# Optimization experiments

Measured on AMD Instinct MI355X. Metric: run time of the kernel, lower is better.

## Reference

```python
import jax, jax.numpy as jnp
import numpy as np

D_MODEL = 1024
NUM_HEADS = 16
HEAD_DIM = D_MODEL // NUM_HEADS
THETA = 10000.0
MAX_SEQ_LEN = 2048
BATCH = 4
SEQ = 2048


def _rope_tables():
    # theta_vec = 1 / theta**(arange(0, d_k, 2)/d_k), pos outer product
    inv_freq = 1.0 / (THETA ** (jnp.arange(0, HEAD_DIM, 2, dtype=jnp.float32) / HEAD_DIM))
    pos = jnp.arange(MAX_SEQ_LEN, dtype=jnp.float32)
    freqs = jnp.outer(pos, inv_freq)  # [max_seq, head_dim//2]
    return jnp.cos(freqs), jnp.sin(freqs)


def apply_rope(x, cos, sin):
    # x: [..., S, d]; cos/sin: [S, d//2]; interleaved pairwise rotation
    x1 = x[..., 0::2]
    x2 = x[..., 1::2]
    o1 = x1 * cos - x2 * sin
    o2 = x2 * cos + x1 * sin
    return jnp.stack([o1, o2], axis=-1).reshape(x.shape)


def setup_inputs() -> dict:
    key = jax.random.key(0)
    kx, kq, kk, kv, ko = jax.random.split(key, 5)
    std = (1.0 / D_MODEL) ** 0.5
    x = jax.random.normal(kx, (BATCH, SEQ, D_MODEL), dtype=jnp.float32)
    w_q = jax.random.normal(kq, (D_MODEL, D_MODEL), dtype=jnp.float32) * std
    w_k = jax.random.normal(kk, (D_MODEL, D_MODEL), dtype=jnp.float32) * std
    w_v = jax.random.normal(kv, (D_MODEL, D_MODEL), dtype=jnp.float32) * std
    w_o = jax.random.normal(ko, (D_MODEL, D_MODEL), dtype=jnp.float32) * std
    cos, sin = _rope_tables()
    return {"x": x, "w_q": w_q, "w_k": w_k, "w_v": w_v, "w_o": w_o,
            "cos": cos, "sin": sin}


def reference(x, w_q, w_k, w_v, w_o, cos, sin):
    b, s, d = x.shape
    h, dk = NUM_HEADS, HEAD_DIM

    def proj(w):
        # einsum '... s d, hd d -> ... s hd' == x @ w.T, then split heads
        y = jnp.einsum('bsd,ed->bse', x, w)
        return y.reshape(b, s, h, dk).transpose(0, 2, 1, 3)  # [b,h,s,dk]

    q = apply_rope(proj(w_q), cos[:s], sin[:s])
    k = apply_rope(proj(w_k), cos[:s], sin[:s])
    v = proj(w_v)

    scores = jnp.einsum('bhnd,bhmd->bhnm', q, k) / (dk ** 0.5)
    causal = jnp.tril(jnp.ones((s, s), dtype=bool))
    scores = jnp.where(causal, scores, -jnp.inf)
    attn = jax.nn.softmax(scores, axis=-1)
    out = jnp.einsum('bhnm,bhmd->bhnd', attn, v)  # [b,h,s,dk]
    out = out.transpose(0, 2, 1, 3).reshape(b, s, d)
    # einsum '... s hd, d hd -> ... s d' == out @ w_o.T
    return jnp.einsum('bse,de->bsd', out, w_o)
```

## Files before the change

### kernel.cpp

```cpp
#include <hip/hip_runtime.h>
#include <hip/hip_bf16.h>


typedef __bf16 bf16;
typedef __bf16 bf16x8 __attribute__((ext_vector_type(8)));
typedef __bf16 bf16x4 __attribute__((ext_vector_type(4)));
typedef float f32x4 __attribute__((ext_vector_type(4)));

#define LOG2E 1.4426950408889634f
#define QSCALE (0.125f * LOG2E * 8388608.0f)
#define SEXP_SEED ((126.94269504f - 16.0f * LOG2E) * 8388608.0f)

__device__ __forceinline__ void async16(const void* g, void* l) {
  __builtin_amdgcn_global_load_lds(
      (const __attribute__((address_space(1))) void*)g,
      (__attribute__((address_space(3))) void*)l, 16, 0, 0);
}

#define MFMA16(a, b, c) __builtin_amdgcn_mfma_f32_16x16x32_bf16(a, b, c, 0, 0, 0)

__global__ void cast_all_kernel(const float* __restrict__ x,
                                const float* __restrict__ wq,
                                const float* __restrict__ wk,
                                const float* __restrict__ wv,
                                const float* __restrict__ wo,
                                const float* __restrict__ cosT,
                                const float* __restrict__ sinT,
                                bf16* __restrict__ xb, bf16* __restrict__ wb,
                                float2* __restrict__ csT) {
  int i = blockIdx.x * blockDim.x + threadIdx.x;
  if (i >= 3145728) {
    int j = i - 3145728;
    float2 cs;
    cs.x = cosT[j];
    cs.y = sinT[j];
    csT[j] = cs;
    return;
  }
  const float* src;
  bf16* dst;
  long o;
  if (i < 2097152) {
    src = x; dst = xb; o = i;
  } else {
    long j = i - 2097152;
    int w = (int)(j >> 18);
    o = j & 262143;
    src = (w == 0) ? wq : (w == 1) ? wk : (w == 2) ? wv : wo;
    dst = wb + (long)w * 1048576;
  }
  float4 v = reinterpret_cast<const float4*>(src)[o];
  bf16x4 out;
  out.x = (bf16)v.x; out.y = (bf16)v.y; out.z = (bf16)v.z; out.w = (bf16)v.w;
  *reinterpret_cast<bf16x4*>(dst + o * 4) = out;
}

template <int EPI, int TM, int TN>
__device__ __forceinline__ void gemm_dev(const bf16* __restrict__ A,
                                         const bf16* __restrict__ B,
                                         void* __restrict__ C, int N, int K,
                                         int bm, int bn, bf16* As, bf16* Bs,
                                         const float2* __restrict__ csT) {
  constexpr int WM = TM / 64;
  constexpr int WN = 4 / WM;
  constexpr int CW = TN / WN;
  constexpr int NT = CW / 16;
  constexpr int ROUNDS = (TM + TN) / 64;
  const int tid = threadIdx.x;
  const int wid = tid >> 6, lane = tid & 63;
  const int quad = lane >> 4, l15 = lane & 15;
  const int waveM = wid / WN, waveN = wid % WN;

  f32x4 acc[4][NT] = {};
  const bf16* Ag = A + (long)bm * TM * K;
  const bf16* Bg = B + (long)bn * TN * K;

  auto stage = [&](int buf, int k0) {
#pragma unroll
    for (int ri = 0; ri < ROUNDS; ++ri) {
      int c = ri * 256 + tid;
      int g = ri * 256 + (wid << 6);
      bool isA = g < TM * 4;
      int cl = isA ? c : c - TM * 4;
      int r = cl >> 2;
      int col = ((cl & 3) ^ ((r >> 1) & 3)) << 3;
      const bf16* src = (isA ? Ag : Bg) + (long)r * K + k0 + col;
      char* dst = isA ? ((char*)As + (long)buf * (TM * 64) + (long)g * 16)
                      : ((char*)Bs + (long)buf * (TN * 64) +
                         (long)(g - TM * 4) * 16);
      async16(src, dst);
    }
  };

  stage(0, 0);
  __syncthreads();
  int cur = 0;
  for (int k0 = 0; k0 < K; k0 += 32) {
    const bool more = (k0 + 32) < K;
    if (more) stage(cur ^ 1, k0 + 32);
    const bf16* Asb = As + cur * (TM * 32);
    const bf16* Bsb = Bs + cur * (TN * 32);
    bf16x8 af[4], bfr[NT];
#pragma unroll
    for (int t = 0; t < 4; ++t) {
      int rowA = waveM * 64 + t * 16 + l15;
      af[t] =
          *(const bf16x8*)(Asb + rowA * 32 + ((quad ^ ((rowA >> 1) & 3)) << 3));
    }
#pragma unroll
    for (int t = 0; t < NT; ++t) {
      int rowB = waveN * CW + t * 16 + l15;
      bfr[t] =
          *(const bf16x8*)(Bsb + rowB * 32 + ((quad ^ ((rowB >> 1) & 3)) << 3));
    }
#pragma unroll
    for (int mt = 0; mt < 4; ++mt)
#pragma unroll
      for (int nt = 0; nt < NT; ++nt)
        acc[mt][nt] = MFMA16(af[mt], bfr[nt], acc[mt][nt]);
    if (more) {
      __syncthreads();
      cur ^= 1;
    }
  }

  const float qsc = (EPI == 0 && bn < 8) ? QSCALE : 1.0f;
#pragma unroll
  for (int mt = 0; mt < 4; ++mt)
#pragma unroll
    for (int nt = 0; nt < NT; ++nt)
#pragma unroll
      for (int r = 0; r < 4; ++r) {
        int row = bm * TM + waveM * 64 + mt * 16 + quad * 4 + r;
        int col = bn * TN + waveN * CW + nt * 16 + l15;
        float v = acc[mt][nt][r];
        if (EPI == 0) {
          float pr = __shfl_xor(v, 1);
          int d = col & 63;
          float2 cs = csT[(row & 2047) * 32 + (d >> 1)];
          float o =
              (col & 1) ? (v * cs.x + pr * cs.y) : (v * cs.x - pr * cs.y);
          o *= qsc;
          long off = (long)(col >> 10) * 8388608 +
                     (long)(((row >> 11) << 4) + ((col >> 6) & 15)) * 131072 +
                     (long)(row & 2047) * 64 + d;
          ((bf16*)C)[off] = (bf16)o;
        } else if (EPI == 1) {
          long off = (long)(col >> 11) * 2097152 + (long)row * 2048 +
                     (col & 2047);
          ((bf16*)C)[off] = (bf16)v;
        } else {
          ((float*)C)[(long)row * N + col] = v;
        }
      }
}

__global__ __launch_bounds__(256) void gemm_qkv(const bf16* __restrict__ xb,
                                                const bf16* __restrict__ wqk,
                                                const bf16* __restrict__ wv,
                                                bf16* __restrict__ QK,
                                                bf16* __restrict__ VT,
                                                const float2* __restrict__ csT) {
  __shared__ __align__(16) bf16 As[2 * 128 * 32];
  __shared__ __align__(16) bf16 Bs[2 * 128 * 32];
  int p = blockIdx.x;
  if (p >= 1024) {
    int pv = p - 1024;
    int lv = (pv & 7) * 128 + (pv >> 3);
    gemm_dev<1, 64, 128>(wv, xb, VT, 8192, 1024, lv & 15, lv >> 4, As, Bs,
                         nullptr);
  } else {
    int l = (p & 7) * 128 + (p >> 3);
    gemm_dev<0, 128, 128>(xb, wqk, QK, 2048, 1024, l >> 4, l & 15, As, Bs,
                          csT);
  }
}

__global__ __launch_bounds__(256) void gemm_out(const bf16* __restrict__ A,
                                                const bf16* __restrict__ B,
                                                float* __restrict__ C) {
  __shared__ __align__(16) bf16 As[2 * 128 * 32];
  __shared__ __align__(16) bf16 Bs[2 * 64 * 32];
  gemm_dev<2, 128, 64>(A, B, C, 1024, 1024, blockIdx.y, blockIdx.x, As, Bs,
                       nullptr);
}

__device__ __forceinline__ void attn_step(const bf16* Ks, const bf16* Vs,
                                          bf16* Pw, const bf16x8* qf,
                                          const bf16x8 ones, f32x4* accO,
                                          f32x4& accL, int quad, int l15,
                                          int qloc, bool diag) {
  const int sw = l15 & 7;
  const f32x4 seedv = {SEXP_SEED, SEXP_SEED, SEXP_SEED, SEXP_SEED};
  f32x4 sacc[4] = {seedv, seedv, seedv, seedv};
#pragma unroll
  for (int mt = 0; mt < 4; ++mt)
#pragma unroll
    for (int kk = 0; kk < 2; ++kk) {
      bf16x8 kf = *(const bf16x8*)(Ks + (mt * 16 + l15) * 64 +
                                   ((((kk << 2) + quad) ^ sw) << 3));
      sacc[mt] = MFMA16(kf, qf[kk], sacc[mt]);
    }
  if (diag) {
#pragma unroll
    for (int mt = 0; mt < 4; ++mt)
#pragma unroll
      for (int r = 0; r < 4; ++r)
        if ((mt * 16 + quad * 4 + r) > qloc) sacc[mt][r] = 0.0f;
  }
#pragma unroll
  for (int mt = 0; mt < 4; ++mt) {
    int i0 = (int)sacc[mt][0], i1 = (int)sacc[mt][1];
    int i2 = (int)sacc[mt][2], i3 = (int)sacc[mt][3];
    uint2 pk;
    pk.x = __builtin_amdgcn_perm((unsigned)i1, (unsigned)i0, 0x07060302u);
    pk.y = __builtin_amdgcn_perm((unsigned)i3, (unsigned)i2, 0x07060302u);
    *(uint2*)(Pw + l15 * 88 + mt * 16 + quad * 4) = pk;
  }
  asm volatile("s_waitcnt lgkmcnt(0)" ::: "memory");
  bf16x8 pfr[2];
#pragma unroll
  for (int kk = 0; kk < 2; ++kk)
    pfr[kk] = *(const bf16x8*)(Pw + l15 * 88 + kk * 32 + quad * 8);
#pragma unroll
  for (int nt = 0; nt < 4; ++nt)
#pragma unroll
    for (int kk = 0; kk < 2; ++kk) {
      bf16x8 vf = *(const bf16x8*)(Vs + (nt * 16 + l15) * 64 +
                                   ((((kk << 2) + quad) ^ sw) << 3));
      accO[nt] = MFMA16(pfr[kk], vf, accO[nt]);
    }
#pragma unroll
  for (int kk = 0; kk < 2; ++kk)
    accL = MFMA16(pfr[kk], ones, accL);
}

__global__ __launch_bounds__(256, 4) void attn_kernel(
    const bf16* __restrict__ Q, const bf16* __restrict__ Kg,
    const bf16* __restrict__ VT, bf16* __restrict__ Out) {
  __shared__ __align__(16) bf16 Ks[64 * 64];
  __shared__ __align__(16) bf16 Vs[64 * 64];
  __shared__ __align__(16) bf16 Ps[4][16 * 88];
  const int tid = threadIdx.x, wid = tid >> 6, lane = tid & 63;
  const int quad = lane >> 4, l15 = lane & 15;
  const int p = blockIdx.x, bh = blockIdx.y;
  const int q0t = p, q1t = 31 - p;
  const bf16* Qb = Q + (long)bh * 131072;
  const bf16* Kb = Kg + (long)bh * 131072;
  const bf16* Vb = VT + (long)bh * 131072;
  bf16* Pw = &Ps[wid][0];
  const int qloc = wid * 16 + l15;

  bf16x8 ones;
#pragma unroll
  for (int j = 0; j < 8; ++j) ones[j] = (bf16)1.0f;

  bf16x8 qf0[2], qf1[2];
#pragma unroll
  for (int kk = 0; kk < 2; ++kk) {
    qf0[kk] = *(const bf16x8*)(Qb + (long)(q0t * 64 + qloc) * 64 + kk * 32 +
                               quad * 8);
    qf1[kk] = *(const bf16x8*)(Qb + (long)(q1t * 64 + qloc) * 64 + kk * 32 +
                               quad * 8);
  }
  f32x4 acc0[4] = {}, acc1[4] = {};
  f32x4 accL0 = {}, accL1 = {};

  for (int kt = 0; kt <= q1t; ++kt) {
#pragma unroll
    for (int it = 0; it < 2; ++it) {
      int chunk = it * 256 + tid;
      int r = chunk >> 3;
      int c = (((chunk & 7) ^ (r & 7)) << 3);
      int ldsbase = (it * 256 + wid * 64) * 16;
      async16(Kb + (long)(kt * 64 + r) * 64 + c, (char*)Ks + ldsbase);
      async16(Vb + (long)r * 2048 + kt * 64 + c, (char*)Vs + ldsbase);
    }
    __syncthreads();
    attn_step(Ks, Vs, Pw, qf1, ones, acc1, accL1, quad, l15, qloc, kt == q1t);
    if (kt <= q0t)
      attn_step(Ks, Vs, Pw, qf0, ones, acc0, accL0, quad, l15, qloc,
                kt == q0t);
    __syncthreads();
  }

  const int b = bh >> 4, h = bh & 15;
#pragma unroll
  for (int r = 0; r < 4; ++r) {
    float lr0 = 1.0f / accL0[r];
    float lr1 = 1.0f / accL1[r];
#pragma unroll
    for (int nt = 0; nt < 4; ++nt) {
      int d = h * 64 + nt * 16 + l15;
      int qg0 = q0t * 64 + wid * 16 + quad * 4 + r;
      int qg1 = q1t * 64 + wid * 16 + quad * 4 + r;
      Out[(long)(b * 2048 + qg0) * 1024 + d] = (bf16)(acc0[nt][r] * lr0);
      Out[(long)(b * 2048 + qg1) * 1024 + d] = (bf16)(acc1[nt][r] * lr1);
    }
  }
}

extern "C" void kernel_launch(void* const* d_in, const int* in_sizes, int n_in,
                              void* d_out, int out_size, void* d_ws,
                              size_t ws_size, hipStream_t stream) {
  const float* x = (const float*)d_in[0];
  const float* w_q = (const float*)d_in[1];
  const float* w_k = (const float*)d_in[2];
  const float* w_v = (const float*)d_in[3];
  const float* w_o = (const float*)d_in[4];
  const float* cosT = (const float*)d_in[5];
  const float* sinT = (const float*)d_in[6];

  char* ws = (char*)d_ws;
  bf16* xb = (bf16*)(ws + 0);
  bf16* wqb = (bf16*)(ws + 16777216);
  bf16* wvb = (bf16*)(ws + 20971520);
  bf16* wob = (bf16*)(ws + 23068672);
  bf16* Qb = (bf16*)(ws + 25165824);
  bf16* Kb = (bf16*)(ws + 41943040);
  bf16* VTb = (bf16*)(ws + 58720256);
  float2* csT = (float2*)(ws + 75497472);
  bf16* attnb = xb;

  cast_all_kernel<<<12544, 256, 0, stream>>>(x, w_q, w_k, w_v, w_o, cosT,
                                             sinT, xb, wqb, csT);

  gemm_qkv<<<2048, 256, 0, stream>>>(xb, wqb, wvb, Qb, VTb, csT);

  attn_kernel<<<dim3(16, 64), 256, 0, stream>>>(Qb, Kb, VTb, attnb);

  gemm_out<<<dim3(16, 64), 256, 0, stream>>>(attnb, wob, (float*)d_out);
}
```

Baseline: 276.0 us.

## Triple-buffer GEMM LDS pipeline with vmcnt waits and retile output GEMM

Moves the shared GEMM mainloop from double to triple buffering. Tiles are prefetched two k-steps ahead, and s_waitcnt vmcnt(N) plus s_barrier replace the full __syncthreads drain, so async global-to-LDS loads overlap more with MFMA work. The output GEMM also switches from 128x64 tiles on a 2D grid to 128x128 tiles with a swizzled 1D block order for better L2 reuse. LDS use rises, which may reduce occupancy, and the hard-coded vmcnt counts depend on ROUNDS matching 3 or 4 outstanding loads per thread.

After: 296.1 us. +7.3%, slower.

```diff
diff --git a/kernel.cpp b/kernel.cpp
--- a/kernel.cpp
+++ b/kernel.cpp
@@ -18,6 +18,16 @@
 }
 
 #define MFMA16(a, b, c) __builtin_amdgcn_mfma_f32_16x16x32_bf16(a, b, c, 0, 0, 0)
+
+template <int N>
+__device__ __forceinline__ void wait_barrier() {
+  if constexpr (N == 0)
+    asm volatile("s_waitcnt vmcnt(0)\n\ts_barrier" ::: "memory");
+  else if constexpr (N == 3)
+    asm volatile("s_waitcnt vmcnt(3)\n\ts_barrier" ::: "memory");
+  else
+    asm volatile("s_waitcnt vmcnt(4)\n\ts_barrier" ::: "memory");
+}
 
 __global__ void cast_all_kernel(const float* __restrict__ x,
                                 const float* __restrict__ wq,
@@ -93,13 +103,16 @@
   };
 
   stage(0, 0);
-  __syncthreads();
-  int cur = 0;
+  stage(1, 32);
+  wait_barrier<ROUNDS>();
+  int bufc = 0;
   for (int k0 = 0; k0 < K; k0 += 32) {
-    const bool more = (k0 + 32) < K;
-    if (more) stage(cur ^ 1, k0 + 32);
-    const bf16* Asb = As + cur * (TM * 32);
-    const bf16* Bsb = Bs + cur * (TN * 32);
+    int nb = bufc + 1; if (nb == 3) nb = 0;
+    int pb = nb + 1; if (pb == 3) pb = 0;
+    const bool more2 = (k0 + 64) < K;
+    if (more2) stage(pb, k0 + 64);
+    const bf16* Asb = As + bufc * (TM * 32);
+    const bf16* Bsb = Bs + bufc * (TN * 32);
     bf16x8 af[4], bfr[NT];
 #pragma unroll
     for (int t = 0; t < 4; ++t) {
@@ -118,10 +131,13 @@
 #pragma unroll
       for (int nt = 0; nt < NT; ++nt)
         acc[mt][nt] = MFMA16(af[mt], bfr[nt], acc[mt][nt]);
-    if (more) {
-      __syncthreads();
-      cur ^= 1;
-    }
+    if (k0 + 32 < K) {
+      if (more2)
+        wait_barrier<ROUNDS>();
+      else
+        wait_barrier<0>();
+    }
+    bufc = nb;
   }
 
   const float qsc = (EPI == 0 && bn < 8) ? QSCALE : 1.0f;
@@ -161,8 +177,8 @@
                                                 bf16* __restrict__ QK,
                                                 bf16* __restrict__ VT,
                                                 const float2* __restrict__ csT) {
-  __shared__ __align__(16) bf16 As[2 * 128 * 32];
-  __shared__ __align__(16) bf16 Bs[2 * 128 * 32];
+  __shared__ __align__(16) bf16 As[3 * 128 * 32];
+  __shared__ __align__(16) bf16 Bs[3 * 128 * 32];
   int p = blockIdx.x;
   if (p >= 1024) {
     int pv = p - 1024;
@@ -179,10 +195,11 @@
 __global__ __launch_bounds__(256) void gemm_out(const bf16* __restrict__ A,
                                                 const bf16* __restrict__ B,
                                                 float* __restrict__ C) {
-  __shared__ __align__(16) bf16 As[2 * 128 * 32];
-  __shared__ __align__(16) bf16 Bs[2 * 64 * 32];
-  gemm_dev<2, 128, 64>(A, B, C, 1024, 1024, blockIdx.y, blockIdx.x, As, Bs,
-                       nullptr);
+  __shared__ __align__(16) bf16 As[3 * 128 * 32];
+  __shared__ __align__(16) bf16 Bs[3 * 128 * 32];
+  int p = blockIdx.x;
+  int l = (p & 7) * 64 + (p >> 3);
+  gemm_dev<2, 128, 128>(A, B, C, 1024, 1024, l >> 3, l & 7, As, Bs, nullptr);
 }
 
 __device__ __forceinline__ void attn_step(const bf16* Ks, const bf16* Vs,
@@ -329,5 +346,5 @@
 
   attn_kernel<<<dim3(16, 64), 256, 0, stream>>>(Qb, Kb, VTb, attnb);
 
-  gemm_out<<<dim3(16, 64), 256, 0, stream>>>(attnb, wob, (float*)d_out);
-}
+  gemm_out<<<512, 256, 0, stream>>>(attnb, wob, (float*)d_out);
+}
```
